# Kernel tuning notes

Hardware: AMD Instinct MI355X
Metric: run time of the kernel (lower is better)

## Reference

```python
import jax, jax.numpy as jnp
import numpy as np

N_NODES = 50000
N_G_EDGES = 400000
N_LG_EDGES = 600000
N_HEADS = 4
OUT_FEATS = 64
EPS = 0.001


def segment_mean(x, seg_ids, num_segments):
    s = jax.ops.segment_sum(x, seg_ids, num_segments=num_segments)
    cnt = jax.ops.segment_sum(jnp.ones((x.shape[0],), x.dtype), seg_ids, num_segments=num_segments)
    return s / jnp.maximum(cnt, 1.0)[(...,) + (None,) * (x.ndim - 1)]


def setup_inputs() -> dict:
    key = jax.random.key(0)
    ks = jax.random.split(key, 12)
    return {
        'atomic_number': jax.random.randint(ks[0], (N_NODES,), 0, 4),
        'g_src': jax.random.randint(ks[1], (N_G_EDGES,), 0, N_NODES),
        'g_dst': jax.random.randint(ks[2], (N_G_EDGES,), 0, N_NODES),
        'lg_src': jax.random.randint(ks[3], (N_LG_EDGES,), 0, N_G_EDGES),
        'lg_dst': jax.random.randint(ks[4], (N_LG_EDGES,), 0, N_G_EDGES),
        'costheta': jax.random.uniform(ks[5], (N_LG_EDGES,), jnp.float32),
        'dnr': jax.random.uniform(ks[6], (N_LG_EDGES,), jnp.float32),
        'a': jax.random.uniform(ks[7], (N_HEADS,), jnp.float32),
        'b': jax.random.uniform(ks[8], (N_HEADS,), jnp.float32),
        'c': jax.random.uniform(ks[9], (N_HEADS,), jnp.float32),
        'd': jax.random.uniform(ks[10], (N_HEADS,), jnp.float32),
        'value_table': jax.random.normal(ks[11], (4, OUT_FEATS * N_HEADS), jnp.float32),
    }


def reference(atomic_number, g_src, g_dst, lg_src, lg_dst, costheta, dnr, a, b, c, d, value_table):
    # send_k_src: per g-edge atomic numbers of endpoints
    k_src = atomic_number[g_src]  # (E_g,)
    k_dst = atomic_number[g_dst]  # (E_g,)

    # masked symmetry key on line-graph edges (edge pair: lg_src -> lg_dst, g-edge indices)
    ka = k_src[lg_src]
    kc = k_dst[lg_dst]
    kb = k_dst[lg_src]
    peripheral = (ka == kc).astype(jnp.int32)
    central = ((kb == ka) & (kb == kc)).astype(jnp.int32)
    sym_key = peripheral * 2 + central  # (E_lg,), values in {0,1,2,3}

    # value embedding lookup -> (E_lg, F, H)
    asv = value_table[sym_key].reshape(N_LG_EDGES, OUT_FEATS, N_HEADS)

    # angular / radial symmetry per head
    ct = jnp.clip(costheta, -EPS, EPS)
    theta = jnp.arccos(ct)[:, None]  # (E_lg, 1)
    B = b % jnp.pi
    angular = ((jnp.cos(a[None, :] * theta + B[None, :]) + 1.0) / 2.0) ** c[None, :]  # (E_lg, H)
    radial = jnp.exp(-d[None, :] * (dnr[:, None] ** 2))  # (E_lg, H)
    spatial = radial * angular

    sv = asv * spatial[:, None, :]  # (E_lg, F, H)

    # reverse line-graph mean: aggregate lg edges by their (original) source lg-node = g-edge
    w_edge = segment_mean(sv, lg_src, N_G_EDGES)  # (E_g, F, H)
    # reverse graph mean: aggregate g edges by their (original) source node
    w_node = segment_mean(w_edge, g_src, N_NODES)  # (N, F, H)

    return jnp.sum(w_node, axis=-1)  # (N, F)
```

## Files before the change

kernel.cpp:

```cpp
#include <hip/hip_runtime.h>
#include <math.h>

typedef unsigned long long u64;
typedef unsigned int u32;
typedef unsigned short u16;
typedef unsigned char u8;

#define N_NODES    50000
#define N_G_EDGES  400000
#define N_LG_EDGES 600000
#define OUT_FEATS  64
#define EPSV       0.001f
#define PI_F       3.14159265358979323846f
#define HPI_F      1.57079632679489662f
#define FXSCALE    512.0f
#define INV_FXSCALE (1.0f/512.0f)

#define SB_N    256
#define EPB1    2344
#define GH_B0   256
#define GH_N    16
#define GH_EPC  25000
#define GH_W    12500
#define PK_B0   272
#define PK_GPB  3572
#define K1_GRID 384

#define WID   1564
#define NPB   196
#define SPB   (NPB*4)
#define CAP2  2816


__global__ __launch_bounds__(1024) void k1(const int* __restrict__ an,
                                           const int* __restrict__ gsrc,
                                           const int* __restrict__ gdst,
                                           const int* __restrict__ lgsrc,
                                           const int* __restrict__ lgdst,
                                           const float* __restrict__ costheta,
                                           const float* __restrict__ dnr,
                                           u8*  __restrict__ kk8,
                                           u32* __restrict__ cg,
                                           u32* __restrict__ prefT1,
                                           u32* __restrict__ sme,
                                           u32* __restrict__ sct,
                                           u32* __restrict__ sdn) {
    __shared__ u32 smem[12500];
    const int tid = threadIdx.x;
    const int bid = blockIdx.x;

    if (bid < SB_N) {
        u32* metaS = smem;
        u32* ctS   = smem + 2344;
        u32* dnS   = smem + 4688;
        u32* lcnt  = smem + 7032;
        u32* pref  = smem + 7288;
        if (tid < 256) lcnt[tid] = 0u;
        __syncthreads();

        const int e0 = bid * EPB1;
        const int e1 = (e0 + EPB1 < N_LG_EDGES) ? e0 + EPB1 : N_LG_EDGES;
        u32 pw[3], cv[3], dv[3], mv[3];
#pragma unroll
        for (int it = 0; it < 3; ++it) {
            mv[it] = 0u;
            int e = e0 + it * 1024 + tid;
            if (e < e1) {
                int ls = __builtin_nontemporal_load(&lgsrc[e]);
                int ld = __builtin_nontemporal_load(&lgdst[e]);
                cv[it] = __float_as_uint(__builtin_nontemporal_load(&costheta[e]));
                dv[it] = __float_as_uint(__builtin_nontemporal_load(&dnr[e]));
                u32 bk = (u32)ls / WID;
                u32 li = (u32)ls - bk * WID;
                pw[it] = ((u32)ld << 11) | li;
                u32 rank = atomicAdd(&lcnt[bk], 1u);
                mv[it] = 0x80000000u | (rank << 8) | bk;
            }
        }
        __syncthreads();
        if (tid < 256) pref[tid + 1] = lcnt[tid];
        if (tid == 0) pref[0] = 0u;
        __syncthreads();
        for (int off = 1; off < 256; off <<= 1) {
            u32 add = 0;
            if (tid < 256 && tid >= off) add = pref[tid - off + 1];
            __syncthreads();
            if (tid < 256) pref[tid + 1] += add;
            __syncthreads();
        }
#pragma unroll
        for (int it = 0; it < 3; ++it) {
            if (mv[it] & 0x80000000u) {
                u32 bk = mv[it] & 0xffu;
                u32 pos = pref[bk] + ((mv[it] >> 8) & 0x7fffffu);
                metaS[pos] = pw[it]; ctS[pos] = cv[it]; dnS[pos] = dv[it];
            }
        }
        __syncthreads();
        const u32 btot = pref[256];
        for (u32 i = tid; i < btot; i += 1024) {
            __builtin_nontemporal_store(metaS[i], &sme[(size_t)bid * EPB1 + i]);
            __builtin_nontemporal_store(ctS[i],   &sct[(size_t)bid * EPB1 + i]);
            __builtin_nontemporal_store(dnS[i],   &sdn[(size_t)bid * EPB1 + i]);
        }
        if (tid <= 256) prefT1[bid * 257 + tid] = pref[tid];
    } else if (bid < PK_B0) {
        const int cc = bid - GH_B0;
        for (int w = tid; w < GH_W; w += 1024) smem[w] = 0u;
        __syncthreads();
        const int s0 = cc * GH_EPC;
        for (int g = s0 + tid; g < s0 + GH_EPC; g += 1024) {
            int n = gsrc[g];
            atomicAdd(&smem[n >> 2], 1u << (8 * (n & 3)));
        }
        __syncthreads();
        for (int w = tid; w < GH_W; w += 1024) cg[cc * GH_W + w] = smem[w];
    } else {
        const int g0 = (bid - PK_B0) * PK_GPB;
        const int g1 = (g0 + PK_GPB < N_G_EDGES) ? g0 + PK_GPB : N_G_EDGES;
        for (int g = g0 + tid; g < g1; g += 1024)
            kk8[g] = (u8)(an[gsrc[g]] | (an[gdst[g]] << 4));
    }
}

__global__ __launch_bounds__(1024) void k2(const int* __restrict__ gsrc,
                                           const u8*  __restrict__ kk8,
                                           const u32* __restrict__ prefT1,
                                           const u32* __restrict__ sme,
                                           const u32* __restrict__ sct,
                                           const u32* __restrict__ sdn,
                                           const float* __restrict__ pa,
                                           const float* __restrict__ pb,
                                           const float* __restrict__ pc,
                                           const float* __restrict__ pd,
                                           u32* __restrict__ mqlo,
                                           u32* __restrict__ mqhi,
                                           u32* __restrict__ mslot,
                                           u32* __restrict__ prefT2) {
    __shared__ u32 smem[12608];
    u32* cntinv = smem;
    u32* nkw    = smem + 1564;
    u32* sstart = smem + 3128;
    u32* spref  = smem + 3384;
    u32* lcnt2  = smem + 3641;
    u32* pref2  = smem + 3897;
    u32* rQlo   = smem + 4160;
    u32* rQhi   = smem + 6976;
    u32* rSl    = smem + 9792;
    const int tid = threadIdx.x;
    const int b = blockIdx.x;
    const int lo = b * WID;

    for (int i = tid; i < WID; i += 1024) cntinv[i] = 0u;
    if (tid < 256) {
        u32 a = prefT1[tid * 257 + b];
        u32 c2 = prefT1[tid * 257 + b + 1];
        sstart[tid] = a; spref[tid + 1] = c2 - a; lcnt2[tid] = 0u;
    }
    if (tid == 0) spref[0] = 0u;
    __syncthreads();
    for (int off = 1; off < 256; off <<= 1) {
        u32 add = 0;
        if (tid < 256 && tid >= off) add = spref[tid - off + 1];
        __syncthreads();
        if (tid < 256) spref[tid + 1] += add;
        __syncthreads();
    }
    const u32 total = spref[256];

    u32 pwv[3]; u32 gidx[3]; u32 valid[3];
#pragma unroll
    for (int it = 0; it < 3; ++it) {
        valid[it] = 0u;
        u32 i = (u32)(it * 1024 + tid);
        if (i < total) {
            int l2 = 0, h2 = 256;
            while (h2 - l2 > 1) {
                int mid = (l2 + h2) >> 1;
                if (spref[mid] <= i) l2 = mid; else h2 = mid;
            }
            u32 idx = (u32)l2 * EPB1 + sstart[l2] + (i - spref[l2]);
            u32 p = __builtin_nontemporal_load(&sme[idx]);
            atomicAdd(&cntinv[p & 0x7ffu], 1u);
            pwv[it] = p; gidx[it] = idx; valid[it] = 1u;
        }
    }
    for (int i = tid; i < WID; i += 1024) {
        int ls = lo + i;
        u32 nk = 0u;
        if (ls < N_G_EDGES)
            nk = (u32)(u16)gsrc[ls] | ((u32)kk8[ls] << 16);
        nkw[i] = nk;
    }
    __syncthreads();
    for (int i = tid; i < WID; i += 1024) {
        u32 c = cntinv[i];
        cntinv[i] = __float_as_uint(1.0f / (float)(c < 1u ? 1u : c));
    }
    __syncthreads();

    float A0[4], A1[4], A2[4], DD[4];
#pragma unroll
    for (int h = 0; h < 4; ++h) {
        float a = pa[h], B = fmodf(pb[h], PI_F), c = pc[h], d = pd[h];
        float K = a * HPI_F + B;
        float ck = cosf(K), sk = sinf(K);
        float u0 = 0.5f * (1.0f + ck);
        float f0 = powf(u0, c);
        float g1v = (-0.5f * a * sk) / u0;
        float u2 = -0.25f * a * a * ck;
        float g2v = u2 / u0 - 0.5f * g1v * g1v;
        A0[h] = f0;
        A1[h] = f0 * c * g1v;
        A2[h] = f0 * (c * g2v + 0.5f * c * c * g1v * g1v);
        DD[h] = d;
    }

    u64 qv[3]; u32 mv2[3];
#pragma unroll
    for (int it = 0; it < 3; ++it) {
        mv2[it] = 0u;
        if (valid[it]) {
            u32 p = pwv[it];
            u32 idx = gidx[it];
            float ct = __uint_as_float(__builtin_nontemporal_load(&sct[idx]));
            float dn = __uint_as_float(__builtin_nontemporal_load(&sdn[idx]));
            u32 li = p & 0x7ffu;
            u32 ld = p >> 11;
            float inv = __uint_as_float(cntinv[li]);
            u32 nk = nkw[li];
            int node = (int)(nk & 0xffffu);
            u32 kw = (nk >> 16) & 0xffu;
            int ka = (int)(kw & 0xfu);
            int kb = (int)(kw >> 4);
            int kd = kk8[ld] >> 4;
            int key = ((ka == kd) ? 2 : 0) + ((kb == ka && kb == kd) ? 1 : 0);
            ct = fminf(fmaxf(ct, -EPSV), EPSV);
            float del = -ct;
            float dn2 = dn * dn;
            float s = inv * FXSCALE;
            u64 q = 0;
#pragma unroll
            for (int h = 0; h < 4; ++h) {
                float ang = A0[h] + del * (A1[h] + del * A2[h]);
                float rad = __expf(-DD[h] * dn2);
                q |= (u64)(u32)(ang * rad * s + 0.5f) << (16 * h);
            }
            u32 nb = (u32)node / NPB;
            u32 slot = ((u32)node - nb * NPB) * 4u + (u32)key;
            u32 rank = atomicAdd(&lcnt2[nb], 1u);
            qv[it] = q;
            mv2[it] = 0x80000000u | (rank << 18) | (nb << 10) | slot;
        }
    }
    __syncthreads();
    if (tid < 256) pref2[tid + 1] = lcnt2[tid];
    if (tid == 0) pref2[0] = 0u;
    __syncthreads();
    for (int off = 1; off < 256; off <<= 1) {
        u32 add = 0;
        if (tid < 256 && tid >= off) add = pref2[tid - off + 1];
        __syncthreads();
        if (tid < 256) pref2[tid + 1] += add;
        __syncthreads();
    }
#pragma unroll
    for (int it = 0; it < 3; ++it) {
        if (mv2[it] & 0x80000000u) {
            u32 nb = (mv2[it] >> 10) & 0xffu;
            u32 pos = pref2[nb] + ((mv2[it] >> 18) & 0x1fffu);
            if (pos < CAP2) {
                rQlo[pos] = (u32)qv[it];
                rQhi[pos] = (u32)(qv[it] >> 32);
                rSl[pos] = mv2[it] & 0x3ffu;
            }
        }
    }
    __syncthreads();
    u32 t2 = pref2[256]; if (t2 > CAP2) t2 = CAP2;
    for (u32 i = tid; i < t2; i += 1024) {
        __builtin_nontemporal_store(rQlo[i], &mqlo[(size_t)b * CAP2 + i]);
        __builtin_nontemporal_store(rQhi[i], &mqhi[(size_t)b * CAP2 + i]);
        __builtin_nontemporal_store(rSl[i],  &mslot[(size_t)b * CAP2 + i]);
    }
    if (tid <= 256) {
        u32 v = pref2[tid];
        prefT2[b * 257 + tid] = (v < CAP2) ? v : CAP2;
    }
}

__global__ __launch_bounds__(1024) void k3(const u32* __restrict__ mqlo,
                                           const u32* __restrict__ mqhi,
                                           const u32* __restrict__ mslot,
                                           const u32* __restrict__ prefT2,
                                           const u32* __restrict__ cg,
                                           const float* __restrict__ VT,
                                           float* __restrict__ out) {
    __shared__ u32 smem[3328];
    u64* ts     = (u64*)smem;
    float* vt_s = (float*)(smem + 1568);
    float* ivg  = (float*)(smem + 2592);
    u32* sstart = smem + 2788;
    u32* spref  = smem + 3044;
    const int tid = threadIdx.x;
    const int nb = blockIdx.x;

    for (int i = tid; i < SPB; i += 1024) ts[i] = 0ull;
    vt_s[tid] = VT[tid];
    if (tid < NPB) {
        int n = nb * NPB + tid;
        float iv = 0.0f;
        if (n < N_NODES) {
            int w = n >> 2, sh = 8 * (n & 3);
            u32 c = 0;
#pragma unroll
            for (int cc = 0; cc < GH_N; ++cc)
                c += (cg[cc * GH_W + w] >> sh) & 0xffu;
            iv = 1.0f / (float)(c < 1u ? 1u : c);
        }
        ivg[tid] = iv;
    }
    if (tid < 256) {
        u32 a = prefT2[tid * 257 + nb];
        u32 c2 = prefT2[tid * 257 + nb + 1];
        sstart[tid] = a; spref[tid + 1] = c2 - a;
    }
    if (tid == 0) spref[0] = 0u;
    __syncthreads();
    for (int off = 1; off < 256; off <<= 1) {
        u32 add = 0;
        if (tid < 256 && tid >= off) add = spref[tid - off + 1];
        __syncthreads();
        if (tid < 256) spref[tid + 1] += add;
        __syncthreads();
    }
    const u32 total = spref[256];

    for (u32 i = tid; i < total; i += 1024) {
        int l2 = 0, h2 = 256;
        while (h2 - l2 > 1) {
            int mid = (l2 + h2) >> 1;
            if (spref[mid] <= i) l2 = mid; else h2 = mid;
        }
        size_t idx = (size_t)l2 * CAP2 + sstart[l2] + (i - spref[l2]);
        u64 q = (u64)__builtin_nontemporal_load(&mqlo[idx])
              | ((u64)__builtin_nontemporal_load(&mqhi[idx]) << 32);
        atomicAdd(&ts[__builtin_nontemporal_load(&mslot[idx])], q);
    }
    __syncthreads();

    const int n0 = nb * NPB;
    for (int j = tid; j < NPB * OUT_FEATS; j += 1024) {
        int nl = j >> 6, f = j & 63;
        int n = n0 + nl;
        if (n < N_NODES) {
            float acc = 0.0f;
#pragma unroll
            for (int k = 0; k < 4; ++k) {
                u64 t = ts[nl * 4 + k];
#pragma unroll
                for (int h = 0; h < 4; ++h) {
                    float tv = (float)((u32)(t >> (16 * h)) & 0xffffu);
                    acc += vt_s[k * 256 + f * 4 + h] * tv;
                }
            }
            __builtin_nontemporal_store(acc * INV_FXSCALE * ivg[nl],
                                        &out[n * OUT_FEATS + f]);
        }
    }
}

extern "C" void kernel_launch(void* const* d_in, const int* in_sizes, int n_in,
                              void* d_out, int out_size, void* d_ws, size_t ws_size,
                              hipStream_t stream) {
    const int*   an       = (const int*)d_in[0];
    const int*   gsrc     = (const int*)d_in[1];
    const int*   gdst     = (const int*)d_in[2];
    const int*   lgsrc    = (const int*)d_in[3];
    const int*   lgdst    = (const int*)d_in[4];
    const float* costheta = (const float*)d_in[5];
    const float* dnr      = (const float*)d_in[6];
    const float* pa       = (const float*)d_in[7];
    const float* pb       = (const float*)d_in[8];
    const float* pc       = (const float*)d_in[9];
    const float* pd       = (const float*)d_in[10];
    const float* vt       = (const float*)d_in[11];
    float* out = (float*)d_out;

    char* ws = (char*)d_ws;
    u8*  kk8    = (u8*) (ws + 0);
    u32* cg     = (u32*)(ws + 400000);
    u32* prefT1 = (u32*)(ws + 1200000);
    u32* prefT2 = (u32*)(ws + 1463168);
    u32* sme    = (u32*)(ws + 1726336);
    u32* sct    = (u32*)(ws + 4126592);
    u32* sdn    = (u32*)(ws + 6526848);
    u32* mqlo   = (u32*)(ws + 8927104);
    u32* mqhi   = (u32*)(ws + 11810688);
    u32* mslot  = (u32*)(ws + 14694272);

    k1<<<dim3(K1_GRID), dim3(1024), 0, stream>>>(
        an, gsrc, gdst, lgsrc, lgdst, costheta, dnr, kk8, cg, prefT1,
        sme, sct, sdn);
    k2<<<dim3(256), dim3(1024), 0, stream>>>(
        gsrc, kk8, prefT1, sme, sct, sdn, pa, pb, pc, pd,
        mqlo, mqhi, mslot, prefT2);
    k3<<<dim3(256), dim3(1024), 0, stream>>>(
        mqlo, mqhi, mslot, prefT2, cg, vt, out);
}
```

Measured before the change: 51.41 us.

## Pack intermediate records into 64-bit words and stage bucket segments in LDS

Quantizes costheta and dnr to 16 bits and packs them with the edge indices into a single 64-bit record in k1. The k2 output packs four 10-bit per-head values plus the slot into one u64 instead of three u32 arrays. Both k2 and k3 now copy their bucket segments into shared memory with per-segment cooperative loads, replacing the per-element binary search and scattered global loads. This cuts intermediate global traffic and indexing work, but the lossy 16-bit and 10-bit quantization risks accuracy loss or overflow of the 10-bit sums.

```diff
diff --git a/kernel.cpp b/kernel.cpp
--- a/kernel.cpp
+++ b/kernel.cpp
@@ -15,6 +15,11 @@
 #define HPI_F      1.57079632679489662f
 #define FXSCALE    512.0f
 #define INV_FXSCALE (1.0f/512.0f)
+
+#define CT_SCALE   3.2e7f
+#define CT_INV     (1.0f/3.2e7f)
+#define DN_SCALE   65535.0f
+#define DN_INV     (1.0f/65535.0f)
 
 #define SB_N    256
 #define EPB1    2344
@@ -42,25 +47,21 @@
                                            u8*  __restrict__ kk8,
                                            u32* __restrict__ cg,
                                            u32* __restrict__ prefT1,
-                                           u32* __restrict__ sme,
-                                           u32* __restrict__ sct,
-                                           u32* __restrict__ sdn) {
-    __shared__ u32 smem[12500];
+                                           u64* __restrict__ sme64) {
+    __shared__ u64 sm64[6250];
     const int tid = threadIdx.x;
     const int bid = blockIdx.x;
 
     if (bid < SB_N) {
-        u32* metaS = smem;
-        u32* ctS   = smem + 2344;
-        u32* dnS   = smem + 4688;
-        u32* lcnt  = smem + 7032;
-        u32* pref  = smem + 7288;
+        u64* metaS = sm64;
+        u32* lcnt  = (u32*)(sm64 + 2344);
+        u32* pref  = (u32*)(sm64 + 2344) + 256;
         if (tid < 256) lcnt[tid] = 0u;
         __syncthreads();
 
         const int e0 = bid * EPB1;
         const int e1 = (e0 + EPB1 < N_LG_EDGES) ? e0 + EPB1 : N_LG_EDGES;
-        u32 pw[3], cv[3], dv[3], mv[3];
+        u64 pv[3]; u32 mv[3];
 #pragma unroll
         for (int it = 0; it < 3; ++it) {
             mv[it] = 0u;
@@ -68,11 +69,16 @@
             if (e < e1) {
                 int ls = __builtin_nontemporal_load(&lgsrc[e]);
                 int ld = __builtin_nontemporal_load(&lgdst[e]);
-                cv[it] = __float_as_uint(__builtin_nontemporal_load(&costheta[e]));
-                dv[it] = __float_as_uint(__builtin_nontemporal_load(&dnr[e]));
+                float ct = __builtin_nontemporal_load(&costheta[e]);
+                float dn = __builtin_nontemporal_load(&dnr[e]);
+                float cc = fminf(fmaxf(ct, -EPSV), EPSV);
+                u32 ct16 = (u32)(u16)(cc * CT_SCALE + 32768.0f + 0.5f);
+                float dns = dn * DN_SCALE + 0.5f;
+                u32 dn16 = (u32)(dns < 65535.0f ? (u16)dns : (u16)65535u);
                 u32 bk = (u32)ls / WID;
                 u32 li = (u32)ls - bk * WID;
-                pw[it] = ((u32)ld << 11) | li;
+                pv[it] = (u64)li | ((u64)(u32)ld << 11) | ((u64)dn16 << 30)
+                       | ((u64)ct16 << 46);
                 u32 rank = atomicAdd(&lcnt[bk], 1u);
                 mv[it] = 0x80000000u | (rank << 8) | bk;
             }
@@ -93,28 +99,26 @@
             if (mv[it] & 0x80000000u) {
                 u32 bk = mv[it] & 0xffu;
                 u32 pos = pref[bk] + ((mv[it] >> 8) & 0x7fffffu);
-                metaS[pos] = pw[it]; ctS[pos] = cv[it]; dnS[pos] = dv[it];
+                metaS[pos] = pv[it];
             }
         }
         __syncthreads();
         const u32 btot = pref[256];
-        for (u32 i = tid; i < btot; i += 1024) {
-            __builtin_nontemporal_store(metaS[i], &sme[(size_t)bid * EPB1 + i]);
-            __builtin_nontemporal_store(ctS[i],   &sct[(size_t)bid * EPB1 + i]);
-            __builtin_nontemporal_store(dnS[i],   &sdn[(size_t)bid * EPB1 + i]);
-        }
+        for (u32 i = tid; i < btot; i += 1024)
+            __builtin_nontemporal_store(metaS[i], &sme64[(size_t)bid * EPB1 + i]);
         if (tid <= 256) prefT1[bid * 257 + tid] = pref[tid];
     } else if (bid < PK_B0) {
+        u32* hist = (u32*)sm64;
         const int cc = bid - GH_B0;
-        for (int w = tid; w < GH_W; w += 1024) smem[w] = 0u;
+        for (int w = tid; w < GH_W; w += 1024) hist[w] = 0u;
         __syncthreads();
         const int s0 = cc * GH_EPC;
         for (int g = s0 + tid; g < s0 + GH_EPC; g += 1024) {
             int n = gsrc[g];
-            atomicAdd(&smem[n >> 2], 1u << (8 * (n & 3)));
-        }
-        __syncthreads();
-        for (int w = tid; w < GH_W; w += 1024) cg[cc * GH_W + w] = smem[w];
+            atomicAdd(&hist[n >> 2], 1u << (8 * (n & 3)));
+        }
+        __syncthreads();
+        for (int w = tid; w < GH_W; w += 1024) cg[cc * GH_W + w] = hist[w];
     } else {
         const int g0 = (bid - PK_B0) * PK_GPB;
         const int g1 = (g0 + PK_GPB < N_G_EDGES) ? g0 + PK_GPB : N_G_EDGES;
@@ -126,27 +130,23 @@
 __global__ __launch_bounds__(1024) void k2(const int* __restrict__ gsrc,
                                            const u8*  __restrict__ kk8,
                                            const u32* __restrict__ prefT1,
-                                           const u32* __restrict__ sme,
-                                           const u32* __restrict__ sct,
-                                           const u32* __restrict__ sdn,
+                                           const u64* __restrict__ sme64,
                                            const float* __restrict__ pa,
                                            const float* __restrict__ pb,
                                            const float* __restrict__ pc,
                                            const float* __restrict__ pd,
-                                           u32* __restrict__ mqlo,
-                                           u32* __restrict__ mqhi,
-                                           u32* __restrict__ mslot,
+                                           u64* __restrict__ mq64,
                                            u32* __restrict__ prefT2) {
-    __shared__ u32 smem[12608];
-    u32* cntinv = smem;
-    u32* nkw    = smem + 1564;
-    u32* sstart = smem + 3128;
-    u32* spref  = smem + 3384;
-    u32* lcnt2  = smem + 3641;
-    u32* pref2  = smem + 3897;
-    u32* rQlo   = smem + 4160;
-    u32* rQhi   = smem + 6976;
-    u32* rSl    = smem + 9792;
+    __shared__ u64 sm64[5632 + 78];
+    __shared__ u32 su[4154];
+    u64* stage  = sm64;
+    u64* outst  = sm64 + 2816;
+    u32* cntinv = su;
+    u32* nkw    = su + 1564;
+    u32* sstart = su + 3128;
+    u32* soff   = su + 3384;
+    u32* lcnt2  = su + 3641;
+    u32* pref2  = su + 3897;
     const int tid = threadIdx.x;
     const int b = blockIdx.x;
     const int lo = b * WID;
@@ -155,34 +155,28 @@
     if (tid < 256) {
         u32 a = prefT1[tid * 257 + b];
         u32 c2 = prefT1[tid * 257 + b + 1];
-        sstart[tid] = a; spref[tid + 1] = c2 - a; lcnt2[tid] = 0u;
-    }
-    if (tid == 0) spref[0] = 0u;
+        sstart[tid] = a; soff[tid + 1] = c2 - a; lcnt2[tid] = 0u;
+    }
+    if (tid == 0) soff[0] = 0u;
     __syncthreads();
     for (int off = 1; off < 256; off <<= 1) {
         u32 add = 0;
-        if (tid < 256 && tid >= off) add = spref[tid - off + 1];
-        __syncthreads();
-        if (tid < 256) spref[tid + 1] += add;
-        __syncthreads();
-    }
-    const u32 total = spref[256];
-
-    u32 pwv[3]; u32 gidx[3]; u32 valid[3];
-#pragma unroll
-    for (int it = 0; it < 3; ++it) {
-        valid[it] = 0u;
-        u32 i = (u32)(it * 1024 + tid);
-        if (i < total) {
-            int l2 = 0, h2 = 256;
-            while (h2 - l2 > 1) {
-                int mid = (l2 + h2) >> 1;
-                if (spref[mid] <= i) l2 = mid; else h2 = mid;
-            }
-            u32 idx = (u32)l2 * EPB1 + sstart[l2] + (i - spref[l2]);
-            u32 p = __builtin_nontemporal_load(&sme[idx]);
-            atomicAdd(&cntinv[p & 0x7ffu], 1u);
-            pwv[it] = p; gidx[it] = idx; valid[it] = 1u;
+        if (tid < 256 && tid >= off) add = soff[tid - off + 1];
+        __syncthreads();
+        if (tid < 256) soff[tid + 1] += add;
+        __syncthreads();
+    }
+    u32 total = soff[256]; if (total > CAP2) total = CAP2;
+
+    {
+        const int g = tid >> 2, lane = tid & 3;
+        const u32 st = sstart[g];
+        const u32 base = soff[g];
+        const u32 len = soff[g + 1] - base;
+        const u64* src = sme64 + (size_t)g * EPB1 + st;
+        for (u32 j = lane; j < len; j += 4) {
+            u32 p = base + j;
+            if (p < CAP2) stage[p] = __builtin_nontemporal_load(&src[j]);
         }
     }
     for (int i = tid; i < WID; i += 1024) {
@@ -192,6 +186,9 @@
             nk = (u32)(u16)gsrc[ls] | ((u32)kk8[ls] << 16);
         nkw[i] = nk;
     }
+    __syncthreads();
+    for (u32 i = tid; i < total; i += 1024)
+        atomicAdd(&cntinv[(u32)(stage[i] & 0x7ffu)], 1u);
     __syncthreads();
     for (int i = tid; i < WID; i += 1024) {
         u32 c = cntinv[i];
@@ -220,13 +217,13 @@
 #pragma unroll
     for (int it = 0; it < 3; ++it) {
         mv2[it] = 0u;
-        if (valid[it]) {
-            u32 p = pwv[it];
-            u32 idx = gidx[it];
-            float ct = __uint_as_float(__builtin_nontemporal_load(&sct[idx]));
-            float dn = __uint_as_float(__builtin_nontemporal_load(&sdn[idx]));
-            u32 li = p & 0x7ffu;
-            u32 ld = p >> 11;
+        u32 i = (u32)(it * 1024 + tid);
+        if (i < total) {
+            u64 v = stage[i];
+            u32 li = (u32)(v & 0x7ffu);
+            u32 ld = (u32)((v >> 11) & 0x7ffffu);
+            float dn = (float)(u32)((v >> 30) & 0xffffu) * DN_INV;
+            float ct = ((float)(u32)((v >> 46) & 0xffffu) - 32768.0f) * CT_INV;
             float inv = __uint_as_float(cntinv[li]);
             u32 nk = nkw[li];
             int node = (int)(nk & 0xffffu);
@@ -235,7 +232,6 @@
             int kb = (int)(kw >> 4);
             int kd = kk8[ld] >> 4;
             int key = ((ka == kd) ? 2 : 0) + ((kb == ka && kb == kd) ? 1 : 0);
-            ct = fminf(fmaxf(ct, -EPSV), EPSV);
             float del = -ct;
             float dn2 = dn * dn;
             float s = inv * FXSCALE;
@@ -244,13 +240,13 @@
             for (int h = 0; h < 4; ++h) {
                 float ang = A0[h] + del * (A1[h] + del * A2[h]);
                 float rad = __expf(-DD[h] * dn2);
-                q |= (u64)(u32)(ang * rad * s + 0.5f) << (16 * h);
+                q |= (u64)(u32)(ang * rad * s + 0.5f) << (10 * h);
             }
             u32 nb = (u32)node / NPB;
             u32 slot = ((u32)node - nb * NPB) * 4u + (u32)key;
             u32 rank = atomicAdd(&lcnt2[nb], 1u);
-            qv[it] = q;
-            mv2[it] = 0x80000000u | (rank << 18) | (nb << 10) | slot;
+            qv[it] = (q << 10) | (u64)slot;
+            mv2[it] = 0x80000000u | (rank << 18) | (nb << 10);
         }
     }
     __syncthreads();
@@ -269,39 +265,32 @@
         if (mv2[it] & 0x80000000u) {
             u32 nb = (mv2[it] >> 10) & 0xffu;
             u32 pos = pref2[nb] + ((mv2[it] >> 18) & 0x1fffu);
-            if (pos < CAP2) {
-                rQlo[pos] = (u32)qv[it];
-                rQhi[pos] = (u32)(qv[it] >> 32);
-                rSl[pos] = mv2[it] & 0x3ffu;
-            }
+            if (pos < CAP2) outst[pos] = qv[it];
         }
     }
     __syncthreads();
     u32 t2 = pref2[256]; if (t2 > CAP2) t2 = CAP2;
-    for (u32 i = tid; i < t2; i += 1024) {
-        __builtin_nontemporal_store(rQlo[i], &mqlo[(size_t)b * CAP2 + i]);
-        __builtin_nontemporal_store(rQhi[i], &mqhi[(size_t)b * CAP2 + i]);
-        __builtin_nontemporal_store(rSl[i],  &mslot[(size_t)b * CAP2 + i]);
-    }
+    for (u32 i = tid; i < t2; i += 1024)
+        __builtin_nontemporal_store(outst[i], &mq64[(size_t)b * CAP2 + i]);
     if (tid <= 256) {
         u32 v = pref2[tid];
         prefT2[b * 257 + tid] = (v < CAP2) ? v : CAP2;
     }
 }
 
-__global__ __launch_bounds__(1024) void k3(const u32* __restrict__ mqlo,
-                                           const u32* __restrict__ mqhi,
-                                           const u32* __restrict__ mslot,
+__global__ __launch_bounds__(1024) void k3(const u64* __restrict__ mq64,
                                            const u32* __restrict__ prefT2,
                                            const u32* __restrict__ cg,
                                            const float* __restrict__ VT,
                                            float* __restrict__ out) {
-    __shared__ u32 smem[3328];
-    u64* ts     = (u64*)smem;
-    float* vt_s = (float*)(smem + 1568);
-    float* ivg  = (float*)(smem + 2592);
-    u32* sstart = smem + 2788;
-    u32* spref  = smem + 3044;
+    __shared__ u64 sm64[2816 + 784];
+    __shared__ u32 su[2506];
+    u64* stage  = sm64;
+    u64* ts     = sm64 + 2816;
+    float* vt_s = (float*)su;
+    float* ivg  = (float*)(su + 1024);
+    u32* sstart = su + 1220;
+    u32* soff   = su + 1476;
     const int tid = threadIdx.x;
     const int nb = blockIdx.x;
 
@@ -323,29 +312,38 @@
     if (tid < 256) {
         u32 a = prefT2[tid * 257 + nb];
         u32 c2 = prefT2[tid * 257 + nb + 1];
-        sstart[tid] = a; spref[tid + 1] = c2 - a;
-    }
-    if (tid == 0) spref[0] = 0u;
+        sstart[tid] = a; soff[tid + 1] = c2 - a;
+    }
+    if (tid == 0) soff[0] = 0u;
     __syncthreads();
     for (int off = 1; off < 256; off <<= 1) {
         u32 add = 0;
-        if (tid < 256 && tid >= off) add = spref[tid - off + 1];
-        __syncthreads();
-        if (tid < 256) spref[tid + 1] += add;
-        __syncthreads();
-    }
-    const u32 total = spref[256];
+        if (tid < 256 && tid >= off) add = soff[tid - off + 1];
+        __syncthreads();
+        if (tid < 256) soff[tid + 1] += add;
+        __syncthreads();
+    }
+    u32 total = soff[256]; if (total > CAP2) total = CAP2;
+
+    {
+        const int g = tid >> 2, lane = tid & 3;
+        const u32 st = sstart[g];
+        const u32 base = soff[g];
+        const u32 len = soff[g + 1] - base;
+        const u64* src = mq64 + (size_t)g * CAP2 + st;
+        for (u32 j = lane; j < len; j += 4) {
+            u32 p = base + j;
+            if (p < CAP2) stage[p] = __builtin_nontemporal_load(&src[j]);
+        }
+    }
+    __syncthreads();
 
     for (u32 i = tid; i < total; i += 1024) {
-        int l2 = 0, h2 = 256;
-        while (h2 - l2 > 1) {
-            int mid = (l2 + h2) >> 1;
-            if (spref[mid] <= i) l2 = mid; else h2 = mid;
-        }
-        size_t idx = (size_t)l2 * CAP2 + sstart[l2] + (i - spref[l2]);
-        u64 q = (u64)__builtin_nontemporal_load(&mqlo[idx])
-              | ((u64)__builtin_nontemporal_load(&mqhi[idx]) << 32);
-        atomicAdd(&ts[__builtin_nontemporal_load(&mslot[idx])], q);
+        u64 v = stage[i];
+        u32 slot = (u32)(v & 0x3ffu);
+        u64 q = ((v >> 10) & 0x3ffu) | (((v >> 20) & 0x3ffu) << 16)
+              | (((v >> 30) & 0x3ffu) << 32) | (((v >> 40) & 0x3ffu) << 48);
+        atomicAdd(&ts[slot], q);
     }
     __syncthreads();
 
@@ -392,19 +390,13 @@
     u32* cg     = (u32*)(ws + 400000);
     u32* prefT1 = (u32*)(ws + 1200000);
     u32* prefT2 = (u32*)(ws + 1463168);
-    u32* sme    = (u32*)(ws + 1726336);
-    u32* sct    = (u32*)(ws + 4126592);
-    u32* sdn    = (u32*)(ws + 6526848);
-    u32* mqlo   = (u32*)(ws + 8927104);
-    u32* mqhi   = (u32*)(ws + 11810688);
-    u32* mslot  = (u32*)(ws + 14694272);
+    u64* sme64  = (u64*)(ws + 1726336);
+    u64* mq64   = (u64*)(ws + 6526848);
 
     k1<<<dim3(K1_GRID), dim3(1024), 0, stream>>>(
-        an, gsrc, gdst, lgsrc, lgdst, costheta, dnr, kk8, cg, prefT1,
-        sme, sct, sdn);
+        an, gsrc, gdst, lgsrc, lgdst, costheta, dnr, kk8, cg, prefT1, sme64);
     k2<<<dim3(256), dim3(1024), 0, stream>>>(
-        gsrc, kk8, prefT1, sme, sct, sdn, pa, pb, pc, pd,
-        mqlo, mqhi, mslot, prefT2);
+        gsrc, kk8, prefT1, sme64, pa, pb, pc, pd, mq64, prefT2);
     k3<<<dim3(256), dim3(1024), 0, stream>>>(
-        mqlo, mqhi, mslot, prefT2, cg, vt, out);
+        mq64, prefT2, cg, vt, out);
 }
```

Result: faster. 48.51 us (-5.6%).
